# Kernel optimization log

Measured on AMD Instinct MI355X. Metric: run time of the kernel, lower is better.

The kernel has to match this reference:

```python
import jax, jax.numpy as jnp
import numpy as np

D_MODEL = 1024
NUM_HEADS = 8
HEAD_DIM = D_MODEL // NUM_HEADS
MAX_SEQ = 10  # module's fixed self.seq_length


def setup_inputs() -> dict:
    key = jax.random.key(0)
    ks = jax.random.split(key, 10)
    B, S, D = 8192, 10, D_MODEL
    sc = 1.0 / np.sqrt(D)
    inp = {
        "x": jax.random.normal(ks[0], (B, S, D), dtype=jnp.float32),
        "Wq": jax.random.normal(ks[1], (D, D), dtype=jnp.float32) * sc,
        "bq": jnp.zeros((D,), dtype=jnp.float32),
        "Wk": jax.random.normal(ks[2], (D, D), dtype=jnp.float32) * sc,
        "bk": jnp.zeros((D,), dtype=jnp.float32),
        "Wv": jax.random.normal(ks[3], (D, D), dtype=jnp.float32) * sc,
        "bv": jnp.zeros((D,), dtype=jnp.float32),
        "Wo": jax.random.normal(ks[4], (D, D), dtype=jnp.float32) * sc,
        "bo": jnp.zeros((D,), dtype=jnp.float32),
        # learned relative position bias, init zeros in torch; use small randn for a nontrivial test
        "pos_bias": jax.random.normal(ks[5], (2 * MAX_SEQ - 1,), dtype=jnp.float32) * 0.02,
    }
    return inp


def reference(x, Wq, bq, Wk, bk, Wv, bv, Wo, bo, pos_bias):
    # x: [B, S, D]; eval mode (dropout = identity)
    B, S, D = x.shape
    H, hd = NUM_HEADS, HEAD_DIM
    scale = hd ** -0.5

    q = (x @ Wq.T + bq).reshape(B, S, H, hd)
    k = (x @ Wk.T + bk).reshape(B, S, H, hd)
    v = (x @ Wv.T + bv).reshape(B, S, H, hd)

    # [B, H, S, S]
    scores = jnp.einsum("bqhd,bkhd->bhqk", q, k) * scale

    # relative position bias (S <= MAX_SEQ)
    rng = jnp.arange(S)
    rel_idx = rng[None, :] - rng[:, None] + S - 1  # [S, S]
    scores = scores + pos_bias[rel_idx][None, None, :, :]

    attn = jax.nn.softmax(scores, axis=-1)
    out = jnp.einsum("bhqk,bkhd->bqhd", attn, v).reshape(B, S, D)
    return out @ Wo.T + bo
```

## Files before the change

### kernel.cpp

```cpp
#include <hip/hip_runtime.h>
#include <hip/hip_bf16.h>
#include <stdint.h>

#define BATCH 8192
#define SEQ   10
#define DM    1024
#define NH    8
#define HD    128
#define MROWS (BATCH*SEQ)

typedef __bf16 bf16x8 __attribute__((ext_vector_type(8)));
typedef float  f32x4  __attribute__((ext_vector_type(4)));

__device__ __forceinline__ unsigned short f2bf(float f) {
  unsigned u = __float_as_uint(f);
  unsigned r = u + 0x7FFFu + ((u >> 16) & 1u);
  return (unsigned short)(r >> 16);
}
__device__ __forceinline__ float bf2f(unsigned short h) {
  return __uint_as_float(((unsigned)h) << 16);
}

__global__ void split_kernel(const float* __restrict__ src,
                             unsigned short* __restrict__ hi,
                             unsigned short* __restrict__ lo, int n4) {
  int i = blockIdx.x * blockDim.x + threadIdx.x;
  int stride = gridDim.x * blockDim.x;
  for (; i < n4; i += stride) {
    float4 v = ((const float4*)src)[i];
    ushort4 h, l;
    h.x = f2bf(v.x); l.x = f2bf(v.x - bf2f(h.x));
    h.y = f2bf(v.y); l.y = f2bf(v.y - bf2f(h.y));
    h.z = f2bf(v.z); l.z = f2bf(v.z - bf2f(h.z));
    h.w = f2bf(v.w); l.w = f2bf(v.w - bf2f(h.w));
    ((ushort4*)hi)[i] = h;
    ((ushort4*)lo)[i] = l;
  }
}

__global__ void pack_bias_kernel(const float* __restrict__ bq, const float* __restrict__ bk,
                                 const float* __restrict__ bv, const float* __restrict__ bo,
                                 float* __restrict__ bias1, float* __restrict__ bias2) {
  int i = blockIdx.x * blockDim.x + threadIdx.x;
  if (i < 1024) {
    bias1[i]        = bq[i];
    bias1[1024 + i] = bk[i];
    bias1[2048 + i] = bv[i];
    bias2[i]        = bo[i];
  }
}

__device__ __forceinline__ void gload_lds16(const void* g, void* l) {
  __builtin_amdgcn_global_load_lds(
      (const __attribute__((address_space(1))) unsigned int*)g,
      (__attribute__((address_space(3))) unsigned int*)l, 16, 0, 0);
}

#define BM 128
#define BN 128
#define BK 32

__global__ __launch_bounds__(256)
void gemm_split_nt(const unsigned short* __restrict__ Ahi,
                   const unsigned short* __restrict__ Alo,
                   const unsigned short* __restrict__ Bhi,
                   const unsigned short* __restrict__ Blo,
                   const float* __restrict__ bias,
                   float* __restrict__ C,
                   int M, int N, int K) {
  __shared__ unsigned short sAh[BM * BK], sAl[BM * BK], sBh[BN * BK], sBl[BN * BK];

  const int tid  = threadIdx.x;
  const int wid  = tid >> 6;
  const int lane = tid & 63;
  const int wr   = wid >> 1, wc = wid & 1;
  const int m0   = blockIdx.y * BM;
  const int n0   = blockIdx.x * BN;

  const f32x4 zero = {0.f, 0.f, 0.f, 0.f};
  f32x4 acc[4][4];
#pragma unroll
  for (int i = 0; i < 4; ++i)
#pragma unroll
    for (int j = 0; j < 4; ++j) acc[i][j] = zero;

  const int off0 = (wid * 2) * 1024 + lane * 16;
  const int off1 = off0 + 1024;
  const int r0c = off0 >> 6, cb0 = off0 & 63;
  const int r1c = off1 >> 6, cb1 = off1 & 63;

  const size_t oA0 = ((size_t)(m0 + r0c) * K) * 2 + cb0;
  const size_t oA1 = ((size_t)(m0 + r1c) * K) * 2 + cb1;
  const size_t oB0 = ((size_t)(n0 + r0c) * K) * 2 + cb0;
  const size_t oB1 = ((size_t)(n0 + r1c) * K) * 2 + cb1;

  const char* pAh = (const char*)Ahi; const char* pAl = (const char*)Alo;
  const char* pBh = (const char*)Bhi; const char* pBl = (const char*)Blo;

  const int fr = lane & 15;
  const int kg = lane >> 4;

  const int nIter = K / BK;
  for (int kt = 0; kt < nIter; ++kt) {
    __syncthreads();
    const size_t kb = (size_t)kt * (BK * 2);
    gload_lds16(pAh + oA0 + kb, (char*)sAh + off0);
    gload_lds16(pAh + oA1 + kb, (char*)sAh + off1);
    gload_lds16(pAl + oA0 + kb, (char*)sAl + off0);
    gload_lds16(pAl + oA1 + kb, (char*)sAl + off1);
    gload_lds16(pBh + oB0 + kb, (char*)sBh + off0);
    gload_lds16(pBh + oB1 + kb, (char*)sBh + off1);
    gload_lds16(pBl + oB0 + kb, (char*)sBl + off0);
    gload_lds16(pBl + oB1 + kb, (char*)sBl + off1);
    __syncthreads();

    bf16x8 a0[4], b0[4], t[4];
#pragma unroll
    for (int mi = 0; mi < 4; ++mi)
      a0[mi] = *(const bf16x8*)(const void*)(sAh + (wr * 64 + mi * 16 + fr) * BK + kg * 8);
#pragma unroll
    for (int ni = 0; ni < 4; ++ni)
      b0[ni] = *(const bf16x8*)(const void*)(sBh + (wc * 64 + ni * 16 + fr) * BK + kg * 8);

#pragma unroll
    for (int mi = 0; mi < 4; ++mi)
#pragma unroll
      for (int ni = 0; ni < 4; ++ni)
        acc[mi][ni] = __builtin_amdgcn_mfma_f32_16x16x32_bf16(a0[mi], b0[ni], acc[mi][ni], 0, 0, 0);

#pragma unroll
    for (int mi = 0; mi < 4; ++mi)
      t[mi] = *(const bf16x8*)(const void*)(sAl + (wr * 64 + mi * 16 + fr) * BK + kg * 8);
#pragma unroll
    for (int mi = 0; mi < 4; ++mi)
#pragma unroll
      for (int ni = 0; ni < 4; ++ni)
        acc[mi][ni] = __builtin_amdgcn_mfma_f32_16x16x32_bf16(t[mi], b0[ni], acc[mi][ni], 0, 0, 0);

#pragma unroll
    for (int ni = 0; ni < 4; ++ni)
      t[ni] = *(const bf16x8*)(const void*)(sBl + (wc * 64 + ni * 16 + fr) * BK + kg * 8);
#pragma unroll
    for (int mi = 0; mi < 4; ++mi)
#pragma unroll
      for (int ni = 0; ni < 4; ++ni)
        acc[mi][ni] = __builtin_amdgcn_mfma_f32_16x16x32_bf16(a0[mi], t[ni], acc[mi][ni], 0, 0, 0);
  }

  const int rq = lane >> 4;
#pragma unroll
  for (int ni = 0; ni < 4; ++ni) {
    const int col = n0 + wc * 64 + ni * 16 + fr;
    const float bb = bias[col];
#pragma unroll
    for (int mi = 0; mi < 4; ++mi) {
      const int row = m0 + wr * 64 + mi * 16 + rq * 4;
#pragma unroll
      for (int j = 0; j < 4; ++j)
        C[(size_t)(row + j) * N + col] = acc[mi][ni][j] + bb;
    }
  }
}

__global__ __launch_bounds__(64)
void attn_kernel(const float* __restrict__ qkv,
                 const float* __restrict__ pos_bias,
                 unsigned short* __restrict__ ao_hi,
                 unsigned short* __restrict__ ao_lo) {
  const int lane = threadIdx.x;
  const int bh = blockIdx.x;
  const int b = bh >> 3, h = bh & 7;
  const float* base = qkv + (size_t)b * (SEQ * 3072) + h * HD + 2 * lane;

  float2 qr[SEQ], kr[SEQ], vr[SEQ];
#pragma unroll
  for (int s = 0; s < SEQ; ++s) {
    qr[s] = *(const float2*)(base + (size_t)s * 3072);
    kr[s] = *(const float2*)(base + (size_t)s * 3072 + 1024);
    vr[s] = *(const float2*)(base + (size_t)s * 3072 + 2048);
  }
  float pb[2 * SEQ - 1];
#pragma unroll
  for (int i = 0; i < 2 * SEQ - 1; ++i) pb[i] = pos_bias[i];

  const float scale = 0.08838834764831845f;

#pragma unroll
  for (int qi = 0; qi < SEQ; ++qi) {
    float srow[SEQ];
#pragma unroll
    for (int kj = 0; kj < SEQ; ++kj) {
      float p = qr[qi].x * kr[kj].x + qr[qi].y * kr[kj].y;
      p += __shfl_xor(p, 32); p += __shfl_xor(p, 16); p += __shfl_xor(p, 8);
      p += __shfl_xor(p, 4);  p += __shfl_xor(p, 2);  p += __shfl_xor(p, 1);
      srow[kj] = p * scale + pb[kj - qi + SEQ - 1];
    }
    float m = srow[0];
#pragma unroll
    for (int kj = 1; kj < SEQ; ++kj) m = fmaxf(m, srow[kj]);
    float sum = 0.f;
#pragma unroll
    for (int kj = 0; kj < SEQ; ++kj) { srow[kj] = expf(srow[kj] - m); sum += srow[kj]; }
    const float inv = 1.f / sum;
    float ax = 0.f, ay = 0.f;
#pragma unroll
    for (int kj = 0; kj < SEQ; ++kj) { ax += srow[kj] * vr[kj].x; ay += srow[kj] * vr[kj].y; }
    ax *= inv; ay *= inv;

    const unsigned short hx = f2bf(ax), hy = f2bf(ay);
    const unsigned short lx = f2bf(ax - bf2f(hx)), ly = f2bf(ay - bf2f(hy));
    const size_t o = ((size_t)b * SEQ + qi) * DM + h * HD + 2 * lane;
    *(unsigned*)(ao_hi + o) = (unsigned)hx | ((unsigned)hy << 16);
    *(unsigned*)(ao_lo + o) = (unsigned)lx | ((unsigned)ly << 16);
  }
}

extern "C" void kernel_launch(void* const* d_in, const int* in_sizes, int n_in,
                              void* d_out, int out_size, void* d_ws, size_t ws_size,
                              hipStream_t stream) {
  const float* x  = (const float*)d_in[0];
  const float* Wq = (const float*)d_in[1];
  const float* bq = (const float*)d_in[2];
  const float* Wk = (const float*)d_in[3];
  const float* bk = (const float*)d_in[4];
  const float* Wv = (const float*)d_in[5];
  const float* bv = (const float*)d_in[6];
  const float* Wo = (const float*)d_in[7];
  const float* bo = (const float*)d_in[8];
  const float* pos_bias = (const float*)d_in[9];
  float* out = (float*)d_out;

  char* p = (char*)d_ws;
  auto alloc = [&](size_t bytes) {
    char* r = p;
    p += (bytes + 255) & ~(size_t)255;
    return r;
  };

  unsigned short* w1h = (unsigned short*)alloc((size_t)3 * DM * DM * 2);
  unsigned short* w1l = (unsigned short*)alloc((size_t)3 * DM * DM * 2);
  unsigned short* w2h = (unsigned short*)alloc((size_t)DM * DM * 2);
  unsigned short* w2l = (unsigned short*)alloc((size_t)DM * DM * 2);
  float* bias1 = (float*)alloc(3072 * 4);
  float* bias2 = (float*)alloc(1024 * 4);

  size_t used = (size_t)(p - (char*)d_ws);
  size_t avail = (ws_size > used + 8192) ? (ws_size - used - 8192) : 0;
  long maxrows = (long)(avail / 16384);
  int cr = (int)((maxrows / 640) * 640);
  if (cr < 640) cr = 640;
  if (cr > MROWS) cr = MROWS;

  unsigned short* xh  = (unsigned short*)alloc((size_t)cr * DM * 2);
  unsigned short* xl  = (unsigned short*)alloc((size_t)cr * DM * 2);
  float*          qkv = (float*)alloc((size_t)cr * 3 * DM * 4);

  split_kernel<<<256, 256, 0, stream>>>(Wq, w1h, w1l, DM * DM / 4);
  split_kernel<<<256, 256, 0, stream>>>(Wk, w1h + DM * DM, w1l + DM * DM, DM * DM / 4);
  split_kernel<<<256, 256, 0, stream>>>(Wv, w1h + 2 * DM * DM, w1l + 2 * DM * DM, DM * DM / 4);
  split_kernel<<<256, 256, 0, stream>>>(Wo, w2h, w2l, DM * DM / 4);
  pack_bias_kernel<<<4, 256, 0, stream>>>(bq, bk, bv, bo, bias1, bias2);

  for (int r0 = 0; r0 < MROWS; r0 += cr) {
    const int m = (MROWS - r0 < cr) ? (MROWS - r0) : cr;
    const int n4 = m * (DM / 4);
    int sgrid = (n4 + 255) / 256; if (sgrid > 2048) sgrid = 2048;

    split_kernel<<<sgrid, 256, 0, stream>>>(x + (size_t)r0 * DM, xh, xl, n4);

    dim3 g1(3 * DM / BN, m / BM);
    gemm_split_nt<<<g1, 256, 0, stream>>>(xh, xl, w1h, w1l, bias1, qkv, m, 3 * DM, DM);

    attn_kernel<<<(m / SEQ) * NH, 64, 0, stream>>>(qkv, pos_bias, xh, xl);

    dim3 g2(DM / BN, m / BM);
    gemm_split_nt<<<g2, 256, 0, stream>>>(xh, xl, w2h, w2l, bias2,
                                          out + (size_t)r0 * DM, m, DM, DM);
  }
}
```

Baseline: 3.277 ms.

## Double-buffer GEMM LDS tiles with XOR swizzle and pack attention heads per block

The split-bf16 GEMM now uses two LDS buffers, so the global-to-LDS loads for the next K tile are issued before the MFMAs on the current tile, and only one barrier per iteration remains. The LDS layout gets an XOR swizzle of the 16-byte chunks to cut bank conflicts on the fragment reads. The attention kernel packs four (batch, head) pairs into each 256-thread block instead of one per 64-thread block, which reduces block launch overhead. Doubling LDS to 64KB per block may lower occupancy.

```diff
diff --git a/kernel.cpp b/kernel.cpp
--- a/kernel.cpp
+++ b/kernel.cpp
@@ -68,7 +68,7 @@
                    const float* __restrict__ bias,
                    float* __restrict__ C,
                    int M, int N, int K) {
-  __shared__ unsigned short sAh[BM * BK], sAl[BM * BK], sBh[BN * BK], sBl[BN * BK];
+  __shared__ char smem[2 * 4 * 8192];
 
   const int tid  = threadIdx.x;
   const int wid  = tid >> 6;
@@ -84,43 +84,60 @@
 #pragma unroll
     for (int j = 0; j < 4; ++j) acc[i][j] = zero;
 
-  const int off0 = (wid * 2) * 1024 + lane * 16;
-  const int off1 = off0 + 1024;
-  const int r0c = off0 >> 6, cb0 = off0 & 63;
-  const int r1c = off1 >> 6, cb1 = off1 & 63;
-
-  const size_t oA0 = ((size_t)(m0 + r0c) * K) * 2 + cb0;
-  const size_t oA1 = ((size_t)(m0 + r1c) * K) * 2 + cb1;
-  const size_t oB0 = ((size_t)(n0 + r0c) * K) * 2 + cb0;
-  const size_t oB1 = ((size_t)(n0 + r1c) * K) * 2 + cb1;
+  const int ldsoff0 = wid * 2048 + lane * 16;
+  const int ldsoff1 = ldsoff0 + 1024;
+  const int ss   = (lane & 3) ^ ((lane >> 2) & 3);
+  const int r0c  = wid * 32 + (lane >> 2);
+  const int r1c  = r0c + 16;
+
+  const size_t bA0 = (size_t)(m0 + r0c) * (K * 2) + ss * 16;
+  const size_t bA1 = (size_t)(m0 + r1c) * (K * 2) + ss * 16;
+  const size_t bB0 = (size_t)(n0 + r0c) * (K * 2) + ss * 16;
+  const size_t bB1 = (size_t)(n0 + r1c) * (K * 2) + ss * 16;
 
   const char* pAh = (const char*)Ahi; const char* pAl = (const char*)Alo;
   const char* pBh = (const char*)Bhi; const char* pBl = (const char*)Blo;
 
-  const int fr = lane & 15;
-  const int kg = lane >> 4;
+  const int fr  = lane & 15;
+  const int kg  = lane >> 4;
+  const int kgs = kg ^ (fr & 3);
 
   const int nIter = K / BK;
+
+#define STAGE(set, kt)                                                        \
+  {                                                                           \
+    char* dst = smem + (set) * 32768;                                         \
+    const size_t kb = (size_t)(kt) * (BK * 2);                                \
+    gload_lds16(pAh + bA0 + kb, dst + ldsoff0);                               \
+    gload_lds16(pAh + bA1 + kb, dst + ldsoff1);                               \
+    gload_lds16(pAl + bA0 + kb, dst + 8192 + ldsoff0);                        \
+    gload_lds16(pAl + bA1 + kb, dst + 8192 + ldsoff1);                        \
+    gload_lds16(pBh + bB0 + kb, dst + 16384 + ldsoff0);                       \
+    gload_lds16(pBh + bB1 + kb, dst + 16384 + ldsoff1);                       \
+    gload_lds16(pBl + bB0 + kb, dst + 24576 + ldsoff0);                       \
+    gload_lds16(pBl + bB1 + kb, dst + 24576 + ldsoff1);                       \
+  }
+
+  STAGE(0, 0);
+  __syncthreads();
+
   for (int kt = 0; kt < nIter; ++kt) {
-    __syncthreads();
-    const size_t kb = (size_t)kt * (BK * 2);
-    gload_lds16(pAh + oA0 + kb, (char*)sAh + off0);
-    gload_lds16(pAh + oA1 + kb, (char*)sAh + off1);
-    gload_lds16(pAl + oA0 + kb, (char*)sAl + off0);
-    gload_lds16(pAl + oA1 + kb, (char*)sAl + off1);
-    gload_lds16(pBh + oB0 + kb, (char*)sBh + off0);
-    gload_lds16(pBh + oB1 + kb, (char*)sBh + off1);
-    gload_lds16(pBl + oB0 + kb, (char*)sBl + off0);
-    gload_lds16(pBl + oB1 + kb, (char*)sBl + off1);
-    __syncthreads();
+    const int cur = kt & 1;
+    if (kt + 1 < nIter) STAGE(cur ^ 1, kt + 1);
+
+    const char* base = smem + cur * 32768;
+    const char* sAh = base;
+    const char* sAl = base + 8192;
+    const char* sBh = base + 16384;
+    const char* sBl = base + 24576;
 
     bf16x8 a0[4], b0[4], t[4];
 #pragma unroll
     for (int mi = 0; mi < 4; ++mi)
-      a0[mi] = *(const bf16x8*)(const void*)(sAh + (wr * 64 + mi * 16 + fr) * BK + kg * 8);
+      a0[mi] = *(const bf16x8*)(sAh + (wr * 64 + mi * 16 + fr) * 64 + kgs * 16);
 #pragma unroll
     for (int ni = 0; ni < 4; ++ni)
-      b0[ni] = *(const bf16x8*)(const void*)(sBh + (wc * 64 + ni * 16 + fr) * BK + kg * 8);
+      b0[ni] = *(const bf16x8*)(sBh + (wc * 64 + ni * 16 + fr) * 64 + kgs * 16);
 
 #pragma unroll
     for (int mi = 0; mi < 4; ++mi)
@@ -130,7 +147,7 @@
 
 #pragma unroll
     for (int mi = 0; mi < 4; ++mi)
-      t[mi] = *(const bf16x8*)(const void*)(sAl + (wr * 64 + mi * 16 + fr) * BK + kg * 8);
+      t[mi] = *(const bf16x8*)(sAl + (wr * 64 + mi * 16 + fr) * 64 + kgs * 16);
 #pragma unroll
     for (int mi = 0; mi < 4; ++mi)
 #pragma unroll
@@ -139,13 +156,16 @@
 
 #pragma unroll
     for (int ni = 0; ni < 4; ++ni)
-      t[ni] = *(const bf16x8*)(const void*)(sBl + (wc * 64 + ni * 16 + fr) * BK + kg * 8);
+      t[ni] = *(const bf16x8*)(sBl + (wc * 64 + ni * 16 + fr) * 64 + kgs * 16);
 #pragma unroll
     for (int mi = 0; mi < 4; ++mi)
 #pragma unroll
       for (int ni = 0; ni < 4; ++ni)
         acc[mi][ni] = __builtin_amdgcn_mfma_f32_16x16x32_bf16(a0[mi], t[ni], acc[mi][ni], 0, 0, 0);
-  }
+
+    __syncthreads();
+  }
+#undef STAGE
 
   const int rq = lane >> 4;
 #pragma unroll
@@ -162,13 +182,13 @@
   }
 }
 
-__global__ __launch_bounds__(64)
+__global__ __launch_bounds__(256)
 void attn_kernel(const float* __restrict__ qkv,
                  const float* __restrict__ pos_bias,
                  unsigned short* __restrict__ ao_hi,
                  unsigned short* __restrict__ ao_lo) {
-  const int lane = threadIdx.x;
-  const int bh = blockIdx.x;
+  const int lane = threadIdx.x & 63;
+  const int bh = blockIdx.x * 4 + (threadIdx.x >> 6);
   const int b = bh >> 3, h = bh & 7;
   const float* base = qkv + (size_t)b * (SEQ * 3072) + h * HD + 2 * lane;
 
@@ -271,7 +291,7 @@
     dim3 g1(3 * DM / BN, m / BM);
     gemm_split_nt<<<g1, 256, 0, stream>>>(xh, xl, w1h, w1l, bias1, qkv, m, 3 * DM, DM);
 
-    attn_kernel<<<(m / SEQ) * NH, 64, 0, stream>>>(qkv, pos_bias, xh, xl);
+    attn_kernel<<<(m / SEQ) * NH / 4, 256, 0, stream>>>(qkv, pos_bias, xh, xl);
 
     dim3 g2(DM / BN, m / BM);
     gemm_split_nt<<<g2, 256, 0, stream>>>(xh, xl, w2h, w2l, bias2,
```

After: 3.028 ms. 1.08x faster.
